# Kernel optimization log

Measured on AMD Instinct MI355X. Metric: run time of the kernel, lower is better.

## Reference

```python
import jax, jax.numpy as jnp
import numpy as np

HEADS = 4
LOCAL_CTX = 8  # local_attn_ctx (stride)


def _strided_transpose(x, n_ctx, local_ctx):
    # [B, n_ctx, E] -> reshape [B, n_ctx//local, local, E] -> swap -> [B, n_ctx, E]
    B, _, E = x.shape
    bT = n_ctx // local_ctx
    return x.reshape(B, bT, local_ctx, E).transpose(0, 2, 1, 3).reshape(B, n_ctx, E)


def _strided_untranspose(a, n_ctx, local_ctx):
    B, _, E = a.shape
    bT = n_ctx // local_ctx
    return a.reshape(B, local_ctx, bT, E).transpose(0, 2, 1, 3).reshape(B, n_ctx, E)


def setup_inputs() -> dict:
    key = jax.random.key(0)
    ks = jax.random.split(key, 6)
    B, T, E = 2048, 64, 256
    value = jax.random.normal(ks[0], (B, T, E), dtype=jnp.float32)
    k_in = jax.random.normal(ks[1], (B, T, E), dtype=jnp.float32)
    query = jax.random.normal(ks[2], (B, T, E), dtype=jnp.float32)
    mask = jnp.ones((B, T), dtype=jnp.int32)  # unused by the block
    W_ff = jax.random.normal(ks[3], (256, T * E), dtype=jnp.float32) * (1.0 / np.sqrt(T * E))
    b_ff = jax.random.normal(ks[4], (256,), dtype=jnp.float32) * 0.01
    return {"value": value, "key": k_in, "query": query, "mask": mask, "W_ff": W_ff, "b_ff": b_ff}


def reference(value, key, query, mask, W_ff, b_ff):
    B, n_ctx, E = query.shape
    # strided transpose of q, k, v
    q = _strided_transpose(query, n_ctx, LOCAL_CTX)
    k = _strided_transpose(key, n_ctx, LOCAL_CTX)
    v = _strided_transpose(value, n_ctx, LOCAL_CTX)
    scale = 1.0 / np.sqrt(E // HEADS)  # n_state = embd // heads
    w = jax.nn.softmax(jnp.einsum('bqe,bke->bqk', q, k) * scale, axis=-1)
    a = jnp.einsum('bqk,bke->bqe', w, v)
    attention = _strided_untranspose(a, n_ctx, LOCAL_CTX)
    # residual + dropout (eval-mode identity)
    x = attention + query
    # flatten-linear + ReLU
    out = jax.nn.relu(x.reshape(B, n_ctx * E) @ W_ff.T + b_ff)
    return (out, attention)
```

## Files before the change

### kernel.cpp

```cpp
#include <hip/hip_runtime.h>
#include <stdint.h>

typedef __attribute__((ext_vector_type(8))) short s16x8;
typedef __attribute__((ext_vector_type(4))) float f32x4;

__device__ __forceinline__ unsigned short f2bf(float f) {
  unsigned int u = __float_as_uint(f);
  u += 0x7fffu + ((u >> 16) & 1u);
  return (unsigned short)(u >> 16);
}
__device__ __forceinline__ float bf2f(unsigned short h) {
  return __uint_as_float(((unsigned int)h) << 16);
}
__device__ __forceinline__ unsigned short hi_trunc(float f) {
  return (unsigned short)(__float_as_uint(f) >> 16);
}
__device__ __forceinline__ f32x4 mfma16(s16x8 a, s16x8 b, f32x4 c) {
  return __builtin_amdgcn_mfma_f32_16x16x32_bf16(a, b, c, 0, 0, 0);
}

__device__ __forceinline__ void write_vq(char* VqB, int ep2, int tg, const float2* g) {
  s16x8 lo, hi;
#pragma unroll
  for (int j = 0; j < 8; ++j) {
    lo[j] = (short)f2bf(g[j].x);
    hi[j] = (short)f2bf(g[j].y);
  }
  *(s16x8*)(VqB + ep2 * 128 + ((16 * tg) ^ (((ep2 >> 1) & 7) << 4))) = lo;
  *(s16x8*)(VqB + (ep2 + 1) * 128 + ((16 * tg) ^ (((ep2 >> 1) & 7) << 4))) = hi;
}

__global__ __launch_bounds__(256) void attn_kernel(
    const float* __restrict__ Vg, const float* __restrict__ Kg,
    const float* __restrict__ Qg, float* __restrict__ attn_out,
    unsigned short* __restrict__ xb ) {
  __shared__ __align__(16) char smem[16384];
  char* VqB = smem;
  char* PLB = smem + 8192;

  const int b = blockIdx.x;
  const int tid = threadIdx.x;
  const int lane = tid & 63;
  const int w = tid >> 6;
  const int n = lane & 15;
  const int q = lane >> 4;

  const float* Qb = Qg + (size_t)b * 64 * 256;
  const float* Kb = Kg + (size_t)b * 64 * 256;
  const float* Vb = Vg + (size_t)b * 64 * 256;

  const int ep2 = (tid & 31) * 2;
  const int tg = tid >> 5;

  f32x4 accS[4];
#pragma unroll
  for (int c = 0; c < 4; ++c) accS[c] = f32x4{0.f, 0.f, 0.f, 0.f};

#pragma unroll
  for (int ph = 0; ph < 2; ++ph) {
    const int e0 = ph * 128;
#pragma unroll
    for (int kk = 0; kk < 4; ++kk) {
      const int cb = kk * 32 + q * 8;
      const float* qsrc = Qb + (16 * w + n) * 256 + e0 + cb;
      float4 q0 = *(const float4*)qsrc;
      float4 q1 = *(const float4*)(qsrc + 4);
      float4 k0[4], k1[4];
#pragma unroll
      for (int c = 0; c < 4; ++c) {
        const float* ksrc = Kb + (16 * c + n) * 256 + e0 + cb;
        k0[c] = *(const float4*)ksrc;
        k1[c] = *(const float4*)(ksrc + 4);
      }
      float qa[8] = {q0.x, q0.y, q0.z, q0.w, q1.x, q1.y, q1.z, q1.w};
      s16x8 qh, ql;
#pragma unroll
      for (int j = 0; j < 8; ++j) {
        unsigned short h = hi_trunc(qa[j]);
        qh[j] = (short)h;
        ql[j] = (short)f2bf(qa[j] - bf2f(h));
      }
#pragma unroll
      for (int c = 0; c < 4; ++c) {
        float ka[8] = {k0[c].x, k0[c].y, k0[c].z, k0[c].w,
                       k1[c].x, k1[c].y, k1[c].z, k1[c].w};
        s16x8 kh, kl;
#pragma unroll
        for (int j = 0; j < 8; ++j) {
          unsigned short h = hi_trunc(ka[j]);
          kh[j] = (short)h;
          kl[j] = (short)f2bf(ka[j] - bf2f(h));
        }
        accS[c] = mfma16(qh, kh, accS[c]);
        accS[c] = mfma16(qh, kl, accS[c]);
        accS[c] = mfma16(ql, kh, accS[c]);
      }
    }
    if (ph == 0) {
    }
  }

  float2 g0[8], g1[8];
#pragma unroll
  for (int j = 0; j < 8; ++j) g0[j] = *(const float2*)(Vb + (tg * 8 + j) * 256 + 0 + ep2);
#pragma unroll
  for (int j = 0; j < 8; ++j) g1[j] = *(const float2*)(Vb + (tg * 8 + j) * 256 + 64 + ep2);

  const float scale = 0.125f;
  float p[4][4];
#pragma unroll
  for (int r = 0; r < 4; ++r) {
    float m = -1e30f;
#pragma unroll
    for (int c = 0; c < 4; ++c) m = fmaxf(m, accS[c][r]);
#pragma unroll
    for (int mk = 1; mk < 16; mk <<= 1) m = fmaxf(m, __shfl_xor(m, mk, 64));
    float s = 0.f;
#pragma unroll
    for (int c = 0; c < 4; ++c) {
      float e = __expf((accS[c][r] - m) * scale);
      p[c][r] = e;
      s += e;
    }
#pragma unroll
    for (int mk = 1; mk < 16; mk <<= 1) s += __shfl_xor(s, mk, 64);
    float inv = 1.0f / s;
#pragma unroll
    for (int c = 0; c < 4; ++c) p[c][r] *= inv;
  }

#pragma unroll
  for (int r = 0; r < 4; ++r) {
    int row = 16 * w + 4 * q + r;
    int sw = (row & 7) << 4;
#pragma unroll
    for (int c = 0; c < 4; ++c)
      *(unsigned short*)(PLB + row * 128 + ((2 * (16 * c + n)) ^ sw)) =
          f2bf(p[c][r]);
  }

  write_vq(VqB, ep2, tg, g0);
  __syncthreads();

  float2 g2[8], g3[8];
#pragma unroll
  for (int qi = 0; qi < 4; ++qi) {
    if (qi == 0) {
#pragma unroll
      for (int j = 0; j < 8; ++j)
        g2[j] = *(const float2*)(Vb + (tg * 8 + j) * 256 + 128 + ep2);
    }
    if (qi == 1) {
#pragma unroll
      for (int j = 0; j < 8; ++j)
        g3[j] = *(const float2*)(Vb + (tg * 8 + j) * 256 + 192 + ep2);
    }

    f32x4 accA[4];
#pragma unroll
    for (int c = 0; c < 4; ++c) accA[c] = f32x4{0.f, 0.f, 0.f, 0.f};
    __builtin_amdgcn_s_setprio(1);
#pragma unroll
    for (int ks = 0; ks < 2; ++ks) {
      const int cb = (ks * 32 + q * 8) * 2;
      s16x8 af = *(const s16x8*)(PLB + (16 * w + n) * 128 + (cb ^ ((n & 7) << 4)));
#pragma unroll
      for (int c = 0; c < 4; ++c) {
        int row = 16 * c + n;
        s16x8 bf = *(const s16x8*)(VqB + row * 128 + (cb ^ (((row >> 1) & 7) << 4)));
        accA[c] = mfma16(af, bf, accA[c]);
      }
    }
    __builtin_amdgcn_s_setprio(0);

#pragma unroll
    for (int r = 0; r < 4; ++r) {
      int t = 16 * w + 4 * q + r;
      const float* qrow = Qb + t * 256 + qi * 64;
      size_t base = ((size_t)b * 64 + t) * 256 + qi * 64;
#pragma unroll
      for (int c = 0; c < 4; ++c) {
        int e = 16 * c + n;
        float aval = accA[c][r];
        attn_out[base + e] = aval;
        if (xb) xb[base + e] = f2bf(aval + qrow[e]);
      }
    }

    if (qi < 3) {
      __syncthreads();
      if (qi == 0) write_vq(VqB, ep2, tg, g1);
      if (qi == 1) write_vq(VqB, ep2, tg, g2);
      if (qi == 2) write_vq(VqB, ep2, tg, g3);
      __syncthreads();
    }
  }
}

__global__ __launch_bounds__(256) void w2b_kernel(const float* __restrict__ W,
                                                  unsigned short* __restrict__ Wb) {
  int i = blockIdx.x * 256 + threadIdx.x;
  float4 v = ((const float4*)W)[i];
  ushort4 o;
  o.x = f2bf(v.x); o.y = f2bf(v.y); o.z = f2bf(v.z); o.w = f2bf(v.w);
  ((ushort4*)Wb)[i] = o;
}

template <bool USE_XB>
__global__ __launch_bounds__(256) void ff_kernel(
    const unsigned short* __restrict__ xb, const float* __restrict__ attn,
    const float* __restrict__ query, const unsigned short* __restrict__ Wb,
    float* __restrict__ part, int kchunk) {
  __shared__ __align__(16) unsigned short As[64 * 72];
  __shared__ __align__(16) unsigned short Bs[64 * 72];
  const int tid = threadIdx.x;
  const int lane = tid & 63, w = tid >> 6, n = lane & 15, q = lane >> 4;
  const int m0 = blockIdx.x * 64;
  const int n0 = blockIdx.y * 64;
  const int k0 = blockIdx.z * kchunk;

  f32x4 acc[4];
#pragma unroll
  for (int c = 0; c < 4; ++c) acc[c] = f32x4{0.f, 0.f, 0.f, 0.f};

  const int srow = tid >> 3;
  const int scol = (tid & 7) * 8;

  for (int kk = 0; kk < kchunk; kk += 64) {
#pragma unroll
    for (int rr = 0; rr < 2; ++rr) {
      int row = rr * 32 + srow;
      size_t ga = (size_t)(m0 + row) * 16384 + k0 + kk + scol;
      if (USE_XB) {
        *(uint4*)(As + row * 72 + scol) = *(const uint4*)(xb + ga);
      } else {
        float4 a0 = *(const float4*)(attn + ga);
        float4 a1 = *(const float4*)(attn + ga + 4);
        float4 q0 = *(const float4*)(query + ga);
        float4 q1 = *(const float4*)(query + ga + 4);
        ushort4 h0, h1;
        h0.x = f2bf(a0.x + q0.x); h0.y = f2bf(a0.y + q0.y);
        h0.z = f2bf(a0.z + q0.z); h0.w = f2bf(a0.w + q0.w);
        h1.x = f2bf(a1.x + q1.x); h1.y = f2bf(a1.y + q1.y);
        h1.z = f2bf(a1.z + q1.z); h1.w = f2bf(a1.w + q1.w);
        *(ushort4*)(As + row * 72 + scol) = h0;
        *(ushort4*)(As + row * 72 + scol + 4) = h1;
      }
      size_t gw = (size_t)(n0 + row) * 16384 + k0 + kk + scol;
      *(uint4*)(Bs + row * 72 + scol) = *(const uint4*)(Wb + gw);
    }
    __syncthreads();
#pragma unroll
    for (int ks = 0; ks < 2; ++ks) {
      const int colb = ks * 32 + q * 8;
      s16x8 af = *(const s16x8*)(As + (16 * w + n) * 72 + colb);
#pragma unroll
      for (int c = 0; c < 4; ++c) {
        s16x8 bf = *(const s16x8*)(Bs + (16 * c + n) * 72 + colb);
        acc[c] = mfma16(af, bf, acc[c]);
      }
    }
    __syncthreads();
  }
#pragma unroll
  for (int r = 0; r < 4; ++r) {
    int m = m0 + 16 * w + 4 * q + r;
#pragma unroll
    for (int c = 0; c < 4; ++c) {
      int nn = n0 + 16 * c + n;
      part[((size_t)blockIdx.z * 2048 + m) * 256 + nn] = acc[c][r];
    }
  }
}

__global__ __launch_bounds__(256) void relu_kernel(const float* __restrict__ part,
                                                   const float* __restrict__ bias,
                                                   float* __restrict__ out, int KS) {
  int idx = blockIdx.x * 256 + threadIdx.x;
  float s = bias[idx & 255];
  for (int ks = 0; ks < KS; ++ks) s += part[(size_t)ks * 2048 * 256 + idx];
  out[idx] = fmaxf(s, 0.f);
}

extern "C" void kernel_launch(void* const* d_in, const int* in_sizes, int n_in,
                              void* d_out, int out_size, void* d_ws, size_t ws_size,
                              hipStream_t stream) {
  const float* value = (const float*)d_in[0];
  const float* key   = (const float*)d_in[1];
  const float* query = (const float*)d_in[2];
  const float* W_ff  = (const float*)d_in[4];
  const float* b_ff  = (const float*)d_in[5];

  float* out  = (float*)d_out;
  float* attn = out + (size_t)2048 * 256;

  const int KS = 4;
  const size_t wb_bytes   = (size_t)256 * 16384 * 2;
  const size_t part_bytes = (size_t)KS * 2048 * 256 * 4;
  const size_t xb_bytes   = (size_t)2048 * 64 * 256 * 2;
  unsigned short* Wb = (unsigned short*)d_ws;
  float* part = (float*)((char*)d_ws + wb_bytes);
  bool use_xb = ws_size >= wb_bytes + part_bytes + xb_bytes;
  unsigned short* xb =
      use_xb ? (unsigned short*)((char*)d_ws + wb_bytes + part_bytes) : nullptr;

  w2b_kernel<<<4096, 256, 0, stream>>>(W_ff, Wb);
  attn_kernel<<<2048, 256, 0, stream>>>(value, key, query, attn, xb);
  dim3 gb(32, 4, KS);
  if (use_xb)
    ff_kernel<true><<<gb, 256, 0, stream>>>(xb, nullptr, nullptr, Wb, part, 16384 / KS);
  else
    ff_kernel<false><<<gb, 256, 0, stream>>>(nullptr, attn, query, Wb, part, 16384 / KS);
  relu_kernel<<<2048, 256, 0, stream>>>(part, b_ff, out, KS);
}
```

Baseline: 292.0 us.

## Switch attention and FF matmuls to fp16 MFMA and double-buffer V staging

Replaces the split-bf16 three-MFMA emulation of the QK^T product with a single fp16 MFMA per tile. All other bf16 conversions (P, V, x, W) move to fp16 as well. V-chunk staging in LDS becomes double-buffered, so the next chunk is written before the output stores and one barrier per iteration is removed. This cuts QK conversion work and MFMA count by roughly 3x and trims synchronisation. The cost is fp16 range and precision: the QK scores lose the hi/lo compensated accuracy, and values beyond fp16 range could overflow.

```diff
diff --git a/kernel.cpp b/kernel.cpp
--- a/kernel.cpp
+++ b/kernel.cpp
@@ -2,29 +2,29 @@
 #include <stdint.h>
 
 typedef __attribute__((ext_vector_type(8))) short s16x8;
+typedef __attribute__((ext_vector_type(8))) _Float16 h16x8;
 typedef __attribute__((ext_vector_type(4))) float f32x4;
 
+__device__ __forceinline__ unsigned short f2h_bits(float f) {
+  union { _Float16 h; unsigned short u; } cv;
+  cv.h = (_Float16)f;
+  return cv.u;
+}
 __device__ __forceinline__ unsigned short f2bf(float f) {
   unsigned int u = __float_as_uint(f);
   u += 0x7fffu + ((u >> 16) & 1u);
   return (unsigned short)(u >> 16);
 }
-__device__ __forceinline__ float bf2f(unsigned short h) {
-  return __uint_as_float(((unsigned int)h) << 16);
-}
-__device__ __forceinline__ unsigned short hi_trunc(float f) {
-  return (unsigned short)(__float_as_uint(f) >> 16);
-}
-__device__ __forceinline__ f32x4 mfma16(s16x8 a, s16x8 b, f32x4 c) {
-  return __builtin_amdgcn_mfma_f32_16x16x32_bf16(a, b, c, 0, 0, 0);
+__device__ __forceinline__ f32x4 mfma16h(h16x8 a, h16x8 b, f32x4 c) {
+  return __builtin_amdgcn_mfma_f32_16x16x32_f16(a, b, c, 0, 0, 0);
 }
 
 __device__ __forceinline__ void write_vq(char* VqB, int ep2, int tg, const float2* g) {
   s16x8 lo, hi;
 #pragma unroll
   for (int j = 0; j < 8; ++j) {
-    lo[j] = (short)f2bf(g[j].x);
-    hi[j] = (short)f2bf(g[j].y);
+    lo[j] = (short)f2h_bits(g[j].x);
+    hi[j] = (short)f2h_bits(g[j].y);
   }
   *(s16x8*)(VqB + ep2 * 128 + ((16 * tg) ^ (((ep2 >> 1) & 7) << 4))) = lo;
   *(s16x8*)(VqB + (ep2 + 1) * 128 + ((16 * tg) ^ (((ep2 >> 1) & 7) << 4))) = hi;
@@ -34,9 +34,8 @@
     const float* __restrict__ Vg, const float* __restrict__ Kg,
     const float* __restrict__ Qg, float* __restrict__ attn_out,
     unsigned short* __restrict__ xb ) {
-  __shared__ __align__(16) char smem[16384];
-  char* VqB = smem;
-  char* PLB = smem + 8192;
+  __shared__ __align__(16) char smem[24576];
+  char* PLB = smem + 16384;
 
   const int b = blockIdx.x;
   const int tid = threadIdx.x;
@@ -72,31 +71,20 @@
         k0[c] = *(const float4*)ksrc;
         k1[c] = *(const float4*)(ksrc + 4);
       }
-      float qa[8] = {q0.x, q0.y, q0.z, q0.w, q1.x, q1.y, q1.z, q1.w};
-      s16x8 qh, ql;
-#pragma unroll
-      for (int j = 0; j < 8; ++j) {
-        unsigned short h = hi_trunc(qa[j]);
-        qh[j] = (short)h;
-        ql[j] = (short)f2bf(qa[j] - bf2f(h));
-      }
-#pragma unroll
-      for (int c = 0; c < 4; ++c) {
-        float ka[8] = {k0[c].x, k0[c].y, k0[c].z, k0[c].w,
-                       k1[c].x, k1[c].y, k1[c].z, k1[c].w};
-        s16x8 kh, kl;
-#pragma unroll
-        for (int j = 0; j < 8; ++j) {
-          unsigned short h = hi_trunc(ka[j]);
-          kh[j] = (short)h;
-          kl[j] = (short)f2bf(ka[j] - bf2f(h));
-        }
-        accS[c] = mfma16(qh, kh, accS[c]);
-        accS[c] = mfma16(qh, kl, accS[c]);
-        accS[c] = mfma16(ql, kh, accS[c]);
-      }
-    }
-    if (ph == 0) {
+      h16x8 qh;
+      qh[0] = (_Float16)q0.x; qh[1] = (_Float16)q0.y;
+      qh[2] = (_Float16)q0.z; qh[3] = (_Float16)q0.w;
+      qh[4] = (_Float16)q1.x; qh[5] = (_Float16)q1.y;
+      qh[6] = (_Float16)q1.z; qh[7] = (_Float16)q1.w;
+#pragma unroll
+      for (int c = 0; c < 4; ++c) {
+        h16x8 kh;
+        kh[0] = (_Float16)k0[c].x; kh[1] = (_Float16)k0[c].y;
+        kh[2] = (_Float16)k0[c].z; kh[3] = (_Float16)k0[c].w;
+        kh[4] = (_Float16)k1[c].x; kh[5] = (_Float16)k1[c].y;
+        kh[6] = (_Float16)k1[c].z; kh[7] = (_Float16)k1[c].w;
+        accS[c] = mfma16h(qh, kh, accS[c]);
+      }
     }
   }
 
@@ -136,15 +124,17 @@
 #pragma unroll
     for (int c = 0; c < 4; ++c)
       *(unsigned short*)(PLB + row * 128 + ((2 * (16 * c + n)) ^ sw)) =
-          f2bf(p[c][r]);
-  }
-
-  write_vq(VqB, ep2, tg, g0);
+          f2h_bits(p[c][r]);
+  }
+
+  write_vq(smem, ep2, tg, g0);
   __syncthreads();
 
   float2 g2[8], g3[8];
+  f32x4 accA[4];
 #pragma unroll
   for (int qi = 0; qi < 4; ++qi) {
+    char* VqB = smem + (qi & 1) * 8192;
     if (qi == 0) {
 #pragma unroll
       for (int j = 0; j < 8; ++j)
@@ -156,22 +146,29 @@
         g3[j] = *(const float2*)(Vb + (tg * 8 + j) * 256 + 192 + ep2);
     }
 
-    f32x4 accA[4];
 #pragma unroll
     for (int c = 0; c < 4; ++c) accA[c] = f32x4{0.f, 0.f, 0.f, 0.f};
     __builtin_amdgcn_s_setprio(1);
 #pragma unroll
     for (int ks = 0; ks < 2; ++ks) {
       const int cb = (ks * 32 + q * 8) * 2;
-      s16x8 af = *(const s16x8*)(PLB + (16 * w + n) * 128 + (cb ^ ((n & 7) << 4)));
+      h16x8 af = *(const h16x8*)(PLB + (16 * w + n) * 128 + (cb ^ ((n & 7) << 4)));
 #pragma unroll
       for (int c = 0; c < 4; ++c) {
         int row = 16 * c + n;
-        s16x8 bf = *(const s16x8*)(VqB + row * 128 + (cb ^ (((row >> 1) & 7) << 4)));
-        accA[c] = mfma16(af, bf, accA[c]);
+        h16x8 bf = *(const h16x8*)(VqB + row * 128 + (cb ^ (((row >> 1) & 7) << 4)));
+        accA[c] = mfma16h(af, bf, accA[c]);
       }
     }
     __builtin_amdgcn_s_setprio(0);
+
+    if (qi < 3) {
+      char* VqN = smem + ((qi + 1) & 1) * 8192;
+      if (qi == 0) write_vq(VqN, ep2, tg, g1);
+      if (qi == 1) write_vq(VqN, ep2, tg, g2);
+      if (qi == 2) write_vq(VqN, ep2, tg, g3);
+      __syncthreads();
+    }
 
 #pragma unroll
     for (int r = 0; r < 4; ++r) {
@@ -183,16 +180,8 @@
         int e = 16 * c + n;
         float aval = accA[c][r];
         attn_out[base + e] = aval;
-        if (xb) xb[base + e] = f2bf(aval + qrow[e]);
-      }
-    }
-
-    if (qi < 3) {
-      __syncthreads();
-      if (qi == 0) write_vq(VqB, ep2, tg, g1);
-      if (qi == 1) write_vq(VqB, ep2, tg, g2);
-      if (qi == 2) write_vq(VqB, ep2, tg, g3);
-      __syncthreads();
+        if (xb) xb[base + e] = f2h_bits(aval + qrow[e]);
+      }
     }
   }
 }
@@ -202,7 +191,7 @@
   int i = blockIdx.x * 256 + threadIdx.x;
   float4 v = ((const float4*)W)[i];
   ushort4 o;
-  o.x = f2bf(v.x); o.y = f2bf(v.y); o.z = f2bf(v.z); o.w = f2bf(v.w);
+  o.x = f2h_bits(v.x); o.y = f2h_bits(v.y); o.z = f2h_bits(v.z); o.w = f2h_bits(v.w);
   ((ushort4*)Wb)[i] = o;
 }
 
@@ -239,10 +228,10 @@
         float4 q0 = *(const float4*)(query + ga);
         float4 q1 = *(const float4*)(query + ga + 4);
         ushort4 h0, h1;
-        h0.x = f2bf(a0.x + q0.x); h0.y = f2bf(a0.y + q0.y);
-        h0.z = f2bf(a0.z + q0.z); h0.w = f2bf(a0.w + q0.w);
-        h1.x = f2bf(a1.x + q1.x); h1.y = f2bf(a1.y + q1.y);
-        h1.z = f2bf(a1.z + q1.z); h1.w = f2bf(a1.w + q1.w);
+        h0.x = f2h_bits(a0.x + q0.x); h0.y = f2h_bits(a0.y + q0.y);
+        h0.z = f2h_bits(a0.z + q0.z); h0.w = f2h_bits(a0.w + q0.w);
+        h1.x = f2h_bits(a1.x + q1.x); h1.y = f2h_bits(a1.y + q1.y);
+        h1.z = f2h_bits(a1.z + q1.z); h1.w = f2h_bits(a1.w + q1.w);
         *(ushort4*)(As + row * 72 + scol) = h0;
         *(ushort4*)(As + row * 72 + scol + 4) = h1;
       }
@@ -253,11 +242,11 @@
 #pragma unroll
     for (int ks = 0; ks < 2; ++ks) {
       const int colb = ks * 32 + q * 8;
-      s16x8 af = *(const s16x8*)(As + (16 * w + n) * 72 + colb);
-#pragma unroll
-      for (int c = 0; c < 4; ++c) {
-        s16x8 bf = *(const s16x8*)(Bs + (16 * c + n) * 72 + colb);
-        acc[c] = mfma16(af, bf, acc[c]);
+      h16x8 af = *(const h16x8*)(As + (16 * w + n) * 72 + colb);
+#pragma unroll
+      for (int c = 0; c < 4; ++c) {
+        h16x8 bf = *(const h16x8*)(Bs + (16 * c + n) * 72 + colb);
+        acc[c] = mfma16h(af, bf, acc[c]);
       }
     }
     __syncthreads();
```

After: 285.6 us. -2.2%, faster.
